# Kernel optimization log

Hardware: AMD Instinct MI355X
Metric: run time of the kernel (lower is better)

## Reference

```python
import jax, jax.numpy as jnp
import numpy as np

N = 100000
E = 1600000
D = 128      # in_features
H = 128      # mlp hidden = out_features
O = 128      # out_features
BN_EPS = 1e-5

def _bn_train(x, gamma, beta):
    # BatchNorm1d in training mode: batch stats over node axis, biased variance
    mu = jnp.mean(x, axis=0)
    var = jnp.mean((x - mu) ** 2, axis=0)
    return (x - mu) * jax.lax.rsqrt(var + BN_EPS) * gamma + beta

def setup_inputs() -> dict:
    key = jax.random.key(0)
    ks = jax.random.split(key, 8)
    h = jax.random.normal(ks[0], (N, D), dtype=jnp.float32)
    edge_src = jax.random.randint(ks[1], (E,), 0, N, dtype=jnp.int32)
    edge_dst = jax.random.randint(ks[2], (E,), 0, N, dtype=jnp.int32)
    s1 = 1.0 / np.sqrt(D)
    s2 = 1.0 / np.sqrt(H)
    W1 = jax.random.uniform(ks[3], (D, H), jnp.float32, -s1, s1)
    b1 = jax.random.uniform(ks[4], (H,), jnp.float32, -s1, s1)
    W2 = jax.random.uniform(ks[5], (H, O), jnp.float32, -s2, s2)
    b2 = jax.random.uniform(ks[6], (O,), jnp.float32, -s2, s2)
    return {
        "h": h, "edge_src": edge_src, "edge_dst": edge_dst,
        "W1": W1, "b1": b1, "g1": jnp.ones((H,), jnp.float32), "be1": jnp.zeros((H,), jnp.float32),
        "W2": W2, "b2": b2, "g2": jnp.ones((O,), jnp.float32), "be2": jnp.zeros((O,), jnp.float32),
        "eps": jnp.zeros((), jnp.float32),
    }

def reference(h, edge_src, edge_dst, W1, b1, g1, be1, W2, b2, g2, be2, eps):
    # spmm(Adj, h) == scatter-add of gathered neighbor features
    msgs = h[edge_src]                                   # [E, D] irregular gather
    pooled = jax.ops.segment_sum(msgs, edge_dst, num_segments=N)  # [N, D]
    pooled = pooled + (1.0 + eps) * h                    # eps combine
    # MLP (2 layers): Linear -> BN -> ReLU -> Linear
    x = jax.nn.relu(_bn_train(pooled @ W1 + b1, g1, be1))
    x = x @ W2 + b2
    # final BN + ReLU
    return jax.nn.relu(_bn_train(x, g2, be2))
```

## Files before the change

### kernel.cpp

```cpp
#include <hip/hip_runtime.h>
#include <hip/hip_bf16.h>
#include <stdint.h>

#define BN_EPS 1e-5f
#define NSTRIPE 64

typedef __attribute__((ext_vector_type(8)))  short bf16x8;
typedef __attribute__((ext_vector_type(16))) float f32x16;

static __device__ __forceinline__ float bflo2f(uint32_t p){
  union { uint32_t u; float f; } c; c.u = p << 16; return c.f;
}
static __device__ __forceinline__ float bfhi2f(uint32_t p){
  union { uint32_t u; float f; } c; c.u = p & 0xffff0000u; return c.f;
}
static __device__ __forceinline__ uint16_t f2bf(float f){
  union { float f; uint32_t u; } c; c.f = f;
  uint32_t u = c.u;
  return (uint16_t)((u + 0x7fffu + ((u >> 16) & 1u)) >> 16);
}
static __device__ __forceinline__ uint32_t pack2(float a, float b){
  return (uint32_t)f2bf(a) | ((uint32_t)f2bf(b) << 16);
}

__global__ void k_prep(const float* __restrict__ h, uint16_t* __restrict__ hb, int hblocks,
                       const float* __restrict__ W1, const float* __restrict__ W2,
                       uint16_t* __restrict__ Wt1, uint16_t* __restrict__ Wt2,
                       float* __restrict__ stats,
                       const int* __restrict__ dst, int* __restrict__ M, int E, int NB){
  int b = blockIdx.x, t = threadIdx.x;
  if (b < hblocks){
    int i = (b * 256 + t) * 8;
    float4 a = *(const float4*)(h + i);
    float4 bb = *(const float4*)(h + i + 4);
    uint4 o;
    o.x = pack2(a.x, a.y); o.y = pack2(a.z, a.w);
    o.z = pack2(bb.x, bb.y); o.w = pack2(bb.z, bb.w);
    *(uint4*)(hb + i) = o;
    return;
  }
  if (b < hblocks + 16){
    int gid = (b - hblocks) * 256 + t;
    {
      float4 z = make_float4(0.f, 0.f, 0.f, 0.f);
      *(float4*)(stats + gid * 8) = z;
      *(float4*)(stats + gid * 8 + 4) = z;
    }
    const float* Wf = (gid < 2048) ? W1 : W2;
    uint16_t* Wt = (gid < 2048) ? Wt1 : Wt2;
    int cid = gid & 2047;
    int nrow = cid >> 4;
    int c    = cid & 15;
    int k0 = c * 8;
    float e[8];
    #pragma unroll
    for (int j = 0; j < 8; ++j) e[j] = Wf[(k0 + j) * 128 + nrow];
    uint4 o;
    o.x = pack2(e[0], e[1]); o.y = pack2(e[2], e[3]);
    o.z = pack2(e[4], e[5]); o.w = pack2(e[6], e[7]);
    *(uint4*)(Wt + nrow * 128 + c * 8) = o;
    return;
  }
  int eb = b - hblocks - 16;
  __shared__ int cnt[512];
  cnt[t] = 0; cnt[t + 256] = 0;
  __syncthreads();
  int base = eb * 4096;
  #pragma unroll 4
  for (int j = t; j < 4096; j += 256){
    int i = base + j;
    if (i < E) atomicAdd(&cnt[dst[i] >> 8], 1);
  }
  __syncthreads();
  size_t row = (size_t)eb * NB;
  if (t < NB) M[row + t] = cnt[t];
  int t2 = t + 256;
  if (t2 < NB) M[row + t2] = cnt[t2];
}

__global__ void k_colscan(int* __restrict__ M, int* __restrict__ btot, int EB, int NB){
  __shared__ int s[256];
  int b = blockIdx.x, t = threadIdx.x;
  int i0 = 2 * t, i1 = 2 * t + 1;
  int v0 = (i0 < EB) ? M[(size_t)i0 * NB + b] : 0;
  int v1 = (i1 < EB) ? M[(size_t)i1 * NB + b] : 0;
  s[t] = v0 + v1;
  __syncthreads();
  for (int off = 1; off < 256; off <<= 1){
    int v = (t >= off) ? s[t - off] : 0;
    __syncthreads();
    s[t] += v;
    __syncthreads();
  }
  int excl = s[t] - (v0 + v1);
  if (i0 < EB) M[(size_t)i0 * NB + b] = excl;
  if (i1 < EB) M[(size_t)i1 * NB + b] = excl + v0;
  if (t == 255) btot[b] = s[255];
}

__global__ void k_bscan(const int* __restrict__ btot, int* __restrict__ bbase,
                        int* __restrict__ row_off, int NB, int n, int E){
  __shared__ int s[256];
  int t = threadIdx.x;
  int i0 = 2 * t, i1 = 2 * t + 1;
  int v0 = (i0 < NB) ? btot[i0] : 0;
  int v1 = (i1 < NB) ? btot[i1] : 0;
  s[t] = v0 + v1;
  __syncthreads();
  for (int off = 1; off < 256; off <<= 1){
    int v = (t >= off) ? s[t - off] : 0;
    __syncthreads();
    s[t] += v;
    __syncthreads();
  }
  int excl = s[t] - (v0 + v1);
  if (i0 < NB) bbase[i0] = excl;
  if (i1 < NB) bbase[i1] = excl + v0;
  if (t == 0){ bbase[NB] = E; row_off[n] = E; }
}

__global__ void k_bin(const int* __restrict__ src, const int* __restrict__ dst,
                      const int* __restrict__ M, const int* __restrict__ bbase,
                      uint2* __restrict__ binned, int E, int NB){
  __shared__ int comb[512];
  __shared__ int cur[512];
  int t = threadIdx.x;
  size_t row = (size_t)blockIdx.x * NB;
  if (t < NB) comb[t] = bbase[t] + M[row + t];
  int t2 = t + 256;
  if (t2 < NB) comb[t2] = bbase[t2] + M[row + t2];
  cur[t] = 0; cur[t + 256] = 0;
  __syncthreads();
  int base = blockIdx.x * 4096;
  #pragma unroll 4
  for (int j = t; j < 4096; j += 256){
    int i = base + j;
    if (i < E){
      int d = dst[i];
      int b = d >> 8;
      int r = atomicAdd(&cur[b], 1);
      binned[comb[b] + r] = make_uint2((unsigned)src[i], (unsigned)d);
    }
  }
}

__global__ void k_csr(const uint2* __restrict__ binned, const int* __restrict__ bbase,
                      int* __restrict__ row_off, int* __restrict__ col_idx, int n){
  __shared__ int cnt[256];
  __shared__ int off[256];
  __shared__ int cur[256];
  int b = blockIdx.x, t = threadIdx.x;
  int e0 = bbase[b], e1 = bbase[b + 1];
  int nb0 = b << 8;
  cnt[t] = 0; cur[t] = 0;
  __syncthreads();
  int m = e1 - e0;
  for (int j = t; j < m; j += 256) atomicAdd(&cnt[binned[e0 + j].y & 255], 1);
  __syncthreads();
  int v = cnt[t];
  off[t] = v;
  __syncthreads();
  for (int o = 1; o < 256; o <<= 1){
    int u = (t >= o) ? off[t - o] : 0;
    __syncthreads();
    off[t] += u;
    __syncthreads();
  }
  int excl = off[t] - v;
  __syncthreads();
  off[t] = excl;
  if (nb0 + t < n) row_off[nb0 + t] = e0 + excl;
  __syncthreads();
  for (int j = t; j < m; j += 256){
    uint2 p = binned[e0 + j];
    int dl = p.y & 255;
    int r = atomicAdd(&cur[dl], 1);
    col_idx[e0 + off[dl] + r] = (int)p.x;
  }
}

__global__ __launch_bounds__(256, 4) void k_gg(
    const uint16_t* __restrict__ hb, const int* __restrict__ row_off,
    const int* __restrict__ col_idx, const float* __restrict__ eps_p,
    const uint16_t* __restrict__ Wt, const float* __restrict__ bias_f,
    uint16_t* __restrict__ Yout, float* __restrict__ osum_s, float* __restrict__ osq_s, int n){
  __shared__ __align__(16) uint16_t Al[64 * 128];
  __shared__ float csum[128], csq[128];
  int tid = threadIdx.x;
  int rbase = blockIdx.x * 64;
  int stripe = blockIdx.x & (NSTRIPE - 1);
  int lane = tid & 63;
  int w    = tid >> 6;
  int g = lane >> 4;
  int c = lane & 15;
  const uint4* hp4 = (const uint4*)hb;
  float ce = 1.0f + eps_p[0];
  if (tid < 128){ csum[tid] = 0.f; csq[tid] = 0.f; }

  for (int it = 0; it < 16; ++it){
    int m = w * 16 + it;
    int gr = rbase + m;
    float a0=0.f,a1=0.f,a2=0.f,a3=0.f,a4=0.f,a5=0.f,a6=0.f,a7=0.f;
    if (gr < n){
      int j = row_off[gr], jend = row_off[gr + 1];
      for (; j + 16 <= jend; j += 16){
        int sA = col_idx[j + g];
        int sB = col_idx[j + 4 + g];
        int sC = col_idx[j + 8 + g];
        int sD = col_idx[j + 12 + g];
        uint4 vA = hp4[(size_t)sA * 16 + c];
        uint4 vB = hp4[(size_t)sB * 16 + c];
        uint4 vC = hp4[(size_t)sC * 16 + c];
        uint4 vD = hp4[(size_t)sD * 16 + c];
        a0 += (bflo2f(vA.x) + bflo2f(vB.x)) + (bflo2f(vC.x) + bflo2f(vD.x));
        a1 += (bfhi2f(vA.x) + bfhi2f(vB.x)) + (bfhi2f(vC.x) + bfhi2f(vD.x));
        a2 += (bflo2f(vA.y) + bflo2f(vB.y)) + (bflo2f(vC.y) + bflo2f(vD.y));
        a3 += (bfhi2f(vA.y) + bfhi2f(vB.y)) + (bfhi2f(vC.y) + bfhi2f(vD.y));
        a4 += (bflo2f(vA.z) + bflo2f(vB.z)) + (bflo2f(vC.z) + bflo2f(vD.z));
        a5 += (bfhi2f(vA.z) + bfhi2f(vB.z)) + (bfhi2f(vC.z) + bfhi2f(vD.z));
        a6 += (bflo2f(vA.w) + bflo2f(vB.w)) + (bflo2f(vC.w) + bflo2f(vD.w));
        a7 += (bfhi2f(vA.w) + bfhi2f(vB.w)) + (bfhi2f(vC.w) + bfhi2f(vD.w));
      }
      for (; j + 4 <= jend; j += 4){
        int s = col_idx[j + g];
        uint4 v = hp4[(size_t)s * 16 + c];
        a0 += bflo2f(v.x); a1 += bfhi2f(v.x);
        a2 += bflo2f(v.y); a3 += bfhi2f(v.y);
        a4 += bflo2f(v.z); a5 += bfhi2f(v.z);
        a6 += bflo2f(v.w); a7 += bfhi2f(v.w);
      }
      int rem = jend - j;
      if (rem > 0){
        int jj = j + (g < rem ? g : rem - 1);
        float wq = (g < rem) ? 1.f : 0.f;
        int s = col_idx[jj];
        uint4 v = hp4[(size_t)s * 16 + c];
        a0 = fmaf(wq, bflo2f(v.x), a0); a1 = fmaf(wq, bfhi2f(v.x), a1);
        a2 = fmaf(wq, bflo2f(v.y), a2); a3 = fmaf(wq, bfhi2f(v.y), a3);
        a4 = fmaf(wq, bflo2f(v.z), a4); a5 = fmaf(wq, bfhi2f(v.z), a5);
        a6 = fmaf(wq, bflo2f(v.w), a6); a7 = fmaf(wq, bfhi2f(v.w), a7);
      }
      a0 += __shfl_xor(a0, 16); a1 += __shfl_xor(a1, 16);
      a2 += __shfl_xor(a2, 16); a3 += __shfl_xor(a3, 16);
      a4 += __shfl_xor(a4, 16); a5 += __shfl_xor(a5, 16);
      a6 += __shfl_xor(a6, 16); a7 += __shfl_xor(a7, 16);
      a0 += __shfl_xor(a0, 32); a1 += __shfl_xor(a1, 32);
      a2 += __shfl_xor(a2, 32); a3 += __shfl_xor(a3, 32);
      a4 += __shfl_xor(a4, 32); a5 += __shfl_xor(a5, 32);
      a6 += __shfl_xor(a6, 32); a7 += __shfl_xor(a7, 32);
      if (g == 0){
        uint4 vh = hp4[(size_t)gr * 16 + c];
        a0 = fmaf(ce, bflo2f(vh.x), a0); a1 = fmaf(ce, bfhi2f(vh.x), a1);
        a2 = fmaf(ce, bflo2f(vh.y), a2); a3 = fmaf(ce, bfhi2f(vh.y), a3);
        a4 = fmaf(ce, bflo2f(vh.z), a4); a5 = fmaf(ce, bfhi2f(vh.z), a5);
        a6 = fmaf(ce, bflo2f(vh.w), a6); a7 = fmaf(ce, bfhi2f(vh.w), a7);
      }
    }
    if (g == 0){
      uint4 o;
      o.x = pack2(a0, a1); o.y = pack2(a2, a3);
      o.z = pack2(a4, a5); o.w = pack2(a6, a7);
      *(uint4*)((char*)Al + m * 256 + ((c ^ (m & 15)) * 16)) = o;
    }
  }
  __syncthreads();

  int hi   = lane >> 5;
  int key  = lane & 15;
  int m0   = (w & 1) * 32;
  int n0   = (w >> 1) * 64;
  int mrow = m0 + (lane & 31);
  int nrow0 = n0 + (lane & 31);
  int nrow1 = nrow0 + 32;

  f32x16 acc0, acc1;
  #pragma unroll
  for (int i = 0; i < 16; ++i){ acc0[i] = 0.f; acc1[i] = 0.f; }

  const char* Ab = (const char*)Al;
  #pragma unroll
  for (int kt = 0; kt < 8; ++kt){
    int ck = 2 * kt + hi;
    bf16x8 a  = *(const bf16x8*)(Ab + mrow * 256 + ((ck ^ key) * 16));
    bf16x8 b0 = *(const bf16x8*)(Wt + nrow0 * 128 + ck * 8);
    bf16x8 b1 = *(const bf16x8*)(Wt + nrow1 * 128 + ck * 8);
    acc0 = __builtin_amdgcn_mfma_f32_32x32x16_bf16(a, b0, acc0, 0, 0, 0);
    acc1 = __builtin_amdgcn_mfma_f32_32x32x16_bf16(a, b1, acc1, 0, 0, 0);
  }
  __syncthreads();

  uint16_t* Yl = Al;
  float bias0 = bias_f[nrow0];
  float bias1 = bias_f[nrow1];
  float ps0 = 0.f, pq0 = 0.f, ps1 = 0.f, pq1 = 0.f;
  #pragma unroll
  for (int r = 0; r < 16; ++r){
    int row = m0 + (r & 3) + 8 * (r >> 2) + 4 * hi;
    bool valid = (rbase + row) < n;
    float y0 = acc0[r] + bias0;
    float y1 = acc1[r] + bias1;
    if (valid){
      ps0 += y0; pq0 += y0 * y0;
      ps1 += y1; pq1 += y1 * y1;
    }
    Yl[row * 128 + nrow0] = f2bf(y0);
    Yl[row * 128 + nrow1] = f2bf(y1);
  }
  atomicAdd(&csum[nrow0], ps0); atomicAdd(&csq[nrow0], pq0);
  atomicAdd(&csum[nrow1], ps1); atomicAdd(&csq[nrow1], pq1);
  __syncthreads();

  #pragma unroll
  for (int i = 0; i < 4; ++i){
    int id = tid + 256 * i;
    int row = id >> 4, cc = id & 15;
    int gr = rbase + row;
    if (gr < n)
      *((uint4*)Yout + (size_t)gr * 16 + cc) = *((const uint4*)Yl + id);
  }
  if (tid < 128){
    atomicAdd(&osum_s[stripe * 128 + tid], csum[tid]);
    atomicAdd(&osq_s[stripe * 128 + tid], csq[tid]);
  }
}

__global__ __launch_bounds__(256, 4) void k_mgemm2(
    const uint16_t* __restrict__ Ag, const uint16_t* __restrict__ Wt,
    const float* __restrict__ bias_f,
    const float* __restrict__ sin_s, const float* __restrict__ sqin_s,
    const float* __restrict__ gin, const float* __restrict__ bein, float invN,
    uint16_t* __restrict__ Yout, float* __restrict__ osum_s, float* __restrict__ osq_s, int n){
  __shared__ __align__(16) uint16_t Al[64 * 128];
  __shared__ float csum[128], csq[128];
  __shared__ __align__(16) float ABl[256];
  int tid = threadIdx.x;
  int rbase = blockIdx.x * 64;
  int stripe = blockIdx.x & (NSTRIPE - 1);

  if (tid < 128){
    float s = 0.f, q = 0.f;
    #pragma unroll 8
    for (int st = 0; st < NSTRIPE; ++st){
      s += sin_s[st * 128 + tid];
      q += sqin_s[st * 128 + tid];
    }
    float mu = s * invN;
    float var = q * invN - mu * mu;
    float A = gin[tid] * rsqrtf(var + BN_EPS);
    ABl[tid] = A;
    ABl[128 + tid] = bein[tid] - mu * A;
    csum[tid] = 0.f; csq[tid] = 0.f;
  }
  __syncthreads();

  #pragma unroll
  for (int i = 0; i < 4; ++i){
    int f = tid + 256 * i;
    int m = f >> 4, c = f & 15;
    int gr = rbase + m;
    uint4 v = make_uint4(0, 0, 0, 0);
    if (gr < n){
      v = *(const uint4*)(Ag + (size_t)gr * 128 + c * 8);
      int k0 = c * 8;
      float4 ka0 = *(const float4*)(ABl + k0);
      float4 ka1 = *(const float4*)(ABl + k0 + 4);
      float4 kb0 = *(const float4*)(ABl + 128 + k0);
      float4 kb1 = *(const float4*)(ABl + 128 + k0 + 4);
      float e0 = fmaxf(fmaf(bflo2f(v.x), ka0.x, kb0.x), 0.f);
      float e1 = fmaxf(fmaf(bfhi2f(v.x), ka0.y, kb0.y), 0.f);
      float e2 = fmaxf(fmaf(bflo2f(v.y), ka0.z, kb0.z), 0.f);
      float e3 = fmaxf(fmaf(bfhi2f(v.y), ka0.w, kb0.w), 0.f);
      float e4 = fmaxf(fmaf(bflo2f(v.z), ka1.x, kb1.x), 0.f);
      float e5 = fmaxf(fmaf(bfhi2f(v.z), ka1.y, kb1.y), 0.f);
      float e6 = fmaxf(fmaf(bflo2f(v.w), ka1.z, kb1.z), 0.f);
      float e7 = fmaxf(fmaf(bfhi2f(v.w), ka1.w, kb1.w), 0.f);
      v.x = pack2(e0, e1); v.y = pack2(e2, e3);
      v.z = pack2(e4, e5); v.w = pack2(e6, e7);
    }
    *(uint4*)((char*)Al + m * 256 + ((c ^ (m & 15)) * 16)) = v;
  }
  __syncthreads();

  int lane = tid & 63;
  int w    = tid >> 6;
  int hi   = lane >> 5;
  int key  = lane & 15;
  int m0   = (w & 1) * 32;
  int n0   = (w >> 1) * 64;
  int mrow = m0 + (lane & 31);
  int nrow0 = n0 + (lane & 31);
  int nrow1 = nrow0 + 32;

  f32x16 acc0, acc1;
  #pragma unroll
  for (int i = 0; i < 16; ++i){ acc0[i] = 0.f; acc1[i] = 0.f; }

  const char* Ab = (const char*)Al;
  #pragma unroll
  for (int kt = 0; kt < 8; ++kt){
    int ck = 2 * kt + hi;
    bf16x8 a  = *(const bf16x8*)(Ab + mrow * 256 + ((ck ^ key) * 16));
    bf16x8 b0 = *(const bf16x8*)(Wt + nrow0 * 128 + ck * 8);
    bf16x8 b1 = *(const bf16x8*)(Wt + nrow1 * 128 + ck * 8);
    acc0 = __builtin_amdgcn_mfma_f32_32x32x16_bf16(a, b0, acc0, 0, 0, 0);
    acc1 = __builtin_amdgcn_mfma_f32_32x32x16_bf16(a, b1, acc1, 0, 0, 0);
  }
  __syncthreads();

  uint16_t* Yl = Al;
  float bias0 = bias_f[nrow0];
  float bias1 = bias_f[nrow1];
  float ps0 = 0.f, pq0 = 0.f, ps1 = 0.f, pq1 = 0.f;
  #pragma unroll
  for (int r = 0; r < 16; ++r){
    int row = m0 + (r & 3) + 8 * (r >> 2) + 4 * hi;
    bool valid = (rbase + row) < n;
    float y0 = acc0[r] + bias0;
    float y1 = acc1[r] + bias1;
    if (valid){
      ps0 += y0; pq0 += y0 * y0;
      ps1 += y1; pq1 += y1 * y1;
    }
    Yl[row * 128 + nrow0] = f2bf(y0);
    Yl[row * 128 + nrow1] = f2bf(y1);
  }
  atomicAdd(&csum[nrow0], ps0); atomicAdd(&csq[nrow0], pq0);
  atomicAdd(&csum[nrow1], ps1); atomicAdd(&csq[nrow1], pq1);
  __syncthreads();

  #pragma unroll
  for (int i = 0; i < 4; ++i){
    int id = tid + 256 * i;
    int row = id >> 4, cc = id & 15;
    int gr = rbase + row;
    if (gr < n)
      *((uint4*)Yout + (size_t)gr * 16 + cc) = *((const uint4*)Yl + id);
  }
  if (tid < 128){
    atomicAdd(&osum_s[stripe * 128 + tid], csum[tid]);
    atomicAdd(&osq_s[stripe * 128 + tid], csq[tid]);
  }
}

__global__ void k_bncoef2(const float* __restrict__ sum_s, const float* __restrict__ sq_s,
                          const float* __restrict__ g, const float* __restrict__ be,
                          float* __restrict__ AB, float invN){
  int c = threadIdx.x;
  if (c < 128){
    float s = 0.f, q = 0.f;
    #pragma unroll 8
    for (int st = 0; st < NSTRIPE; ++st){
      s += sum_s[st * 128 + c];
      q += sq_s[st * 128 + c];
    }
    float mu = s * invN;
    float var = q * invN - mu * mu;
    float A = g[c] * rsqrtf(var + BN_EPS);
    AB[c] = A;
    AB[128 + c] = be[c] - mu * A;
  }
}

__global__ void k_final(const uint16_t* __restrict__ Y2b, const float* __restrict__ ABg,
                        float* __restrict__ out, int total){
  __shared__ __align__(16) float AB[256];
  int tid = threadIdx.x;
  if (tid < 64){
    *(float4*)(AB + tid * 4) = *(const float4*)(ABg + tid * 4);
  }
  __syncthreads();
  int i = (blockIdx.x * 256 + tid) * 4;
  if (i >= total) return;
  uint2 v = *(const uint2*)(Y2b + i);
  int c = i & 127;
  float4 a = *(const float4*)(AB + c);
  float4 b = *(const float4*)(AB + 128 + c);
  float4 o;
  o.x = fmaxf(fmaf(bflo2f(v.x), a.x, b.x), 0.f);
  o.y = fmaxf(fmaf(bfhi2f(v.x), a.y, b.y), 0.f);
  o.z = fmaxf(fmaf(bflo2f(v.y), a.z, b.z), 0.f);
  o.w = fmaxf(fmaf(bfhi2f(v.y), a.w, b.w), 0.f);
  *(float4*)(out + i) = o;
}

extern "C" void kernel_launch(void* const* d_in, const int* in_sizes, int n_in,
                              void* d_out, int out_size, void* d_ws, size_t ws_size,
                              hipStream_t stream){
  const float* h    = (const float*)d_in[0];
  const int*   esrc = (const int*)d_in[1];
  const int*   edst = (const int*)d_in[2];
  const float* W1   = (const float*)d_in[3];
  const float* b1   = (const float*)d_in[4];
  const float* g1   = (const float*)d_in[5];
  const float* be1  = (const float*)d_in[6];
  const float* W2   = (const float*)d_in[7];
  const float* b2   = (const float*)d_in[8];
  const float* g2   = (const float*)d_in[9];
  const float* be2  = (const float*)d_in[10];
  const float* eps  = (const float*)d_in[11];
  int n = in_sizes[0] / 128;
  int E = in_sizes[1];
  (void)n_in; (void)out_size; (void)ws_size;

  int NB = (n + 255) >> 8;
  int EB = (E + 4095) >> 12;

  char* ws = (char*)d_ws;
  size_t off = 0;
  auto alloc = [&](size_t bytes) -> void* {
    void* p = ws + off;
    off += (bytes + 511) & ~(size_t)511;
    return p;
  };
  size_t feat_b = (size_t)n * 128 * 2;
  uint16_t* B1   = (uint16_t*)alloc(feat_b);
  uint16_t* B2   = (uint16_t*)alloc(feat_b);
  int*   row_off = (int*)alloc((size_t)(n + 1) * 4);
  int*   col_idx = (int*)alloc((size_t)E * 4);
  int*   M       = (int*)alloc((size_t)EB * NB * 4);
  int*   btot    = (int*)alloc((size_t)(NB + 1) * 4);
  int*   bbase   = (int*)alloc((size_t)(NB + 1) * 4);
  float* stats   = (float*)alloc((size_t)4 * NSTRIPE * 128 * 4);
  float* AB2     = (float*)alloc(256 * 4);
  uint16_t* Wt1  = (uint16_t*)alloc(128 * 128 * 2);
  uint16_t* Wt2  = (uint16_t*)alloc(128 * 128 * 2);
  float* sum1 = stats;
  float* sq1  = stats + NSTRIPE * 128;
  float* sum2 = stats + 2 * NSTRIPE * 128;
  float* sq2  = stats + 3 * NSTRIPE * 128;
  uint16_t* hb  = B1;
  uint2*   binned = (uint2*)B2;
  uint16_t* Y1b = B2;
  uint16_t* Y2b = B1;

  int total = n * 128;
  int hblocks = total / 8 / 256;
  float invN = 1.0f / (float)n;

  k_prep<<<hblocks + 16 + EB, 256, 0, stream>>>(h, hb, hblocks, W1, W2, Wt1, Wt2,
                                                stats, edst, M, E, NB);
  k_colscan<<<NB, 256, 0, stream>>>(M, btot, EB, NB);
  k_bscan  <<<1, 256, 0, stream>>>(btot, bbase, row_off, NB, n, E);
  k_bin    <<<EB, 256, 0, stream>>>(esrc, edst, M, bbase, binned, E, NB);
  k_csr    <<<NB, 256, 0, stream>>>(binned, bbase, row_off, col_idx, n);

  int gblocks = (n + 63) / 64;
  k_gg<<<gblocks, 256, 0, stream>>>(hb, row_off, col_idx, eps, Wt1, b1,
                                    Y1b, sum1, sq1, n);
  k_mgemm2<<<gblocks, 256, 0, stream>>>(Y1b, Wt2, b2,
      sum1, sq1, g1, be1, invN, Y2b, sum2, sq2, n);

  k_bncoef2<<<1, 128, 0, stream>>>(sum2, sq2, g2, be2, AB2, invN);
  k_final<<<(total / 4 + 255) / 256, 256, 0, stream>>>(Y2b, AB2, (float*)d_out, total);
}
```

Before: 305.2 us.

## Pack binned edges into 32-bit words and assign one 16-lane group per row

The binned edge array now packs the source index (24 bits) and the low 8 bits of the destination into one 32-bit word instead of a uint2, halving the binning write and CSR read traffic. The gather kernel now gives each 16-lane group its own destination row, so 16 rows are in flight per block iteration instead of 4. Each group issues eight independent row gathers per loop step, and the cross-group shuffle reduction and g==0 predication are gone. In exchange, all 16 lanes load the same col_idx entries redundantly, and rows with fewer edges leave lanes idle in the masked tail. The 24-bit packing limits node count to 16M.

```diff
diff --git a/kernel.cpp b/kernel.cpp
--- a/kernel.cpp
+++ b/kernel.cpp
@@ -121,7 +121,7 @@
 
 __global__ void k_bin(const int* __restrict__ src, const int* __restrict__ dst,
                       const int* __restrict__ M, const int* __restrict__ bbase,
-                      uint2* __restrict__ binned, int E, int NB){
+                      uint32_t* __restrict__ binned, int E, int NB){
   __shared__ int comb[512];
   __shared__ int cur[512];
   int t = threadIdx.x;
@@ -139,12 +139,12 @@
       int d = dst[i];
       int b = d >> 8;
       int r = atomicAdd(&cur[b], 1);
-      binned[comb[b] + r] = make_uint2((unsigned)src[i], (unsigned)d);
-    }
-  }
-}
-
-__global__ void k_csr(const uint2* __restrict__ binned, const int* __restrict__ bbase,
+      binned[comb[b] + r] = (uint32_t)src[i] | ((uint32_t)(d & 255) << 24);
+    }
+  }
+}
+
+__global__ void k_csr(const uint32_t* __restrict__ binned, const int* __restrict__ bbase,
                       int* __restrict__ row_off, int* __restrict__ col_idx, int n){
   __shared__ int cnt[256];
   __shared__ int off[256];
@@ -155,7 +155,7 @@
   cnt[t] = 0; cur[t] = 0;
   __syncthreads();
   int m = e1 - e0;
-  for (int j = t; j < m; j += 256) atomicAdd(&cnt[binned[e0 + j].y & 255], 1);
+  for (int j = t; j < m; j += 256) atomicAdd(&cnt[binned[e0 + j] >> 24], 1);
   __syncthreads();
   int v = cnt[t];
   off[t] = v;
@@ -172,10 +172,10 @@
   if (nb0 + t < n) row_off[nb0 + t] = e0 + excl;
   __syncthreads();
   for (int j = t; j < m; j += 256){
-    uint2 p = binned[e0 + j];
-    int dl = p.y & 255;
+    uint32_t p = binned[e0 + j];
+    int dl = (int)(p >> 24);
     int r = atomicAdd(&cur[dl], 1);
-    col_idx[e0 + off[dl] + r] = (int)p.x;
+    col_idx[e0 + off[dl] + r] = (int)(p & 0xFFFFFFu);
   }
 }
 
@@ -189,82 +189,67 @@
   int tid = threadIdx.x;
   int rbase = blockIdx.x * 64;
   int stripe = blockIdx.x & (NSTRIPE - 1);
-  int lane = tid & 63;
-  int w    = tid >> 6;
-  int g = lane >> 4;
-  int c = lane & 15;
+  int grp = tid >> 4;
+  int c   = tid & 15;
   const uint4* hp4 = (const uint4*)hb;
   float ce = 1.0f + eps_p[0];
   if (tid < 128){ csum[tid] = 0.f; csq[tid] = 0.f; }
 
-  for (int it = 0; it < 16; ++it){
-    int m = w * 16 + it;
+  for (int it = 0; it < 4; ++it){
+    int m = it * 16 + grp;
     int gr = rbase + m;
     float a0=0.f,a1=0.f,a2=0.f,a3=0.f,a4=0.f,a5=0.f,a6=0.f,a7=0.f;
     if (gr < n){
       int j = row_off[gr], jend = row_off[gr + 1];
-      for (; j + 16 <= jend; j += 16){
-        int sA = col_idx[j + g];
-        int sB = col_idx[j + 4 + g];
-        int sC = col_idx[j + 8 + g];
-        int sD = col_idx[j + 12 + g];
-        uint4 vA = hp4[(size_t)sA * 16 + c];
-        uint4 vB = hp4[(size_t)sB * 16 + c];
-        uint4 vC = hp4[(size_t)sC * 16 + c];
-        uint4 vD = hp4[(size_t)sD * 16 + c];
-        a0 += (bflo2f(vA.x) + bflo2f(vB.x)) + (bflo2f(vC.x) + bflo2f(vD.x));
-        a1 += (bfhi2f(vA.x) + bfhi2f(vB.x)) + (bfhi2f(vC.x) + bfhi2f(vD.x));
-        a2 += (bflo2f(vA.y) + bflo2f(vB.y)) + (bflo2f(vC.y) + bflo2f(vD.y));
-        a3 += (bfhi2f(vA.y) + bfhi2f(vB.y)) + (bfhi2f(vC.y) + bfhi2f(vD.y));
-        a4 += (bflo2f(vA.z) + bflo2f(vB.z)) + (bflo2f(vC.z) + bflo2f(vD.z));
-        a5 += (bfhi2f(vA.z) + bfhi2f(vB.z)) + (bfhi2f(vC.z) + bfhi2f(vD.z));
-        a6 += (bflo2f(vA.w) + bflo2f(vB.w)) + (bflo2f(vC.w) + bflo2f(vD.w));
-        a7 += (bfhi2f(vA.w) + bfhi2f(vB.w)) + (bfhi2f(vC.w) + bfhi2f(vD.w));
+      for (; j + 8 <= jend; j += 8){
+        int s[8];
+        #pragma unroll
+        for (int e = 0; e < 8; ++e) s[e] = col_idx[j + e];
+        uint4 v[8];
+        #pragma unroll
+        for (int e = 0; e < 8; ++e) v[e] = hp4[(size_t)s[e] * 16 + c];
+        #pragma unroll
+        for (int e = 0; e < 8; ++e){
+          a0 += bflo2f(v[e].x); a1 += bfhi2f(v[e].x);
+          a2 += bflo2f(v[e].y); a3 += bfhi2f(v[e].y);
+          a4 += bflo2f(v[e].z); a5 += bfhi2f(v[e].z);
+          a6 += bflo2f(v[e].w); a7 += bfhi2f(v[e].w);
+        }
       }
-      for (; j + 4 <= jend; j += 4){
-        int s = col_idx[j + g];
-        uint4 v = hp4[(size_t)s * 16 + c];
-        a0 += bflo2f(v.x); a1 += bfhi2f(v.x);
-        a2 += bflo2f(v.y); a3 += bfhi2f(v.y);
-        a4 += bflo2f(v.z); a5 += bfhi2f(v.z);
-        a6 += bflo2f(v.w); a7 += bfhi2f(v.w);
+      if (j < jend){
+        int s[8]; float wq[8];
+        #pragma unroll
+        for (int e = 0; e < 8; ++e){
+          int jj = j + e;
+          wq[e] = (jj < jend) ? 1.f : 0.f;
+          s[e] = col_idx[(jj < jend) ? jj : (jend - 1)];
+        }
+        uint4 v[8];
+        #pragma unroll
+        for (int e = 0; e < 8; ++e) v[e] = hp4[(size_t)s[e] * 16 + c];
+        #pragma unroll
+        for (int e = 0; e < 8; ++e){
+          a0 = fmaf(wq[e], bflo2f(v[e].x), a0); a1 = fmaf(wq[e], bfhi2f(v[e].x), a1);
+          a2 = fmaf(wq[e], bflo2f(v[e].y), a2); a3 = fmaf(wq[e], bfhi2f(v[e].y), a3);
+          a4 = fmaf(wq[e], bflo2f(v[e].z), a4); a5 = fmaf(wq[e], bfhi2f(v[e].z), a5);
+          a6 = fmaf(wq[e], bflo2f(v[e].w), a6); a7 = fmaf(wq[e], bfhi2f(v[e].w), a7);
+        }
       }
-      int rem = jend - j;
-      if (rem > 0){
-        int jj = j + (g < rem ? g : rem - 1);
-        float wq = (g < rem) ? 1.f : 0.f;
-        int s = col_idx[jj];
-        uint4 v = hp4[(size_t)s * 16 + c];
-        a0 = fmaf(wq, bflo2f(v.x), a0); a1 = fmaf(wq, bfhi2f(v.x), a1);
-        a2 = fmaf(wq, bflo2f(v.y), a2); a3 = fmaf(wq, bfhi2f(v.y), a3);
-        a4 = fmaf(wq, bflo2f(v.z), a4); a5 = fmaf(wq, bfhi2f(v.z), a5);
-        a6 = fmaf(wq, bflo2f(v.w), a6); a7 = fmaf(wq, bfhi2f(v.w), a7);
-      }
-      a0 += __shfl_xor(a0, 16); a1 += __shfl_xor(a1, 16);
-      a2 += __shfl_xor(a2, 16); a3 += __shfl_xor(a3, 16);
-      a4 += __shfl_xor(a4, 16); a5 += __shfl_xor(a5, 16);
-      a6 += __shfl_xor(a6, 16); a7 += __shfl_xor(a7, 16);
-      a0 += __shfl_xor(a0, 32); a1 += __shfl_xor(a1, 32);
-      a2 += __shfl_xor(a2, 32); a3 += __shfl_xor(a3, 32);
-      a4 += __shfl_xor(a4, 32); a5 += __shfl_xor(a5, 32);
-      a6 += __shfl_xor(a6, 32); a7 += __shfl_xor(a7, 32);
-      if (g == 0){
-        uint4 vh = hp4[(size_t)gr * 16 + c];
-        a0 = fmaf(ce, bflo2f(vh.x), a0); a1 = fmaf(ce, bfhi2f(vh.x), a1);
-        a2 = fmaf(ce, bflo2f(vh.y), a2); a3 = fmaf(ce, bfhi2f(vh.y), a3);
-        a4 = fmaf(ce, bflo2f(vh.z), a4); a5 = fmaf(ce, bfhi2f(vh.z), a5);
-        a6 = fmaf(ce, bflo2f(vh.w), a6); a7 = fmaf(ce, bfhi2f(vh.w), a7);
-      }
-    }
-    if (g == 0){
-      uint4 o;
-      o.x = pack2(a0, a1); o.y = pack2(a2, a3);
-      o.z = pack2(a4, a5); o.w = pack2(a6, a7);
-      *(uint4*)((char*)Al + m * 256 + ((c ^ (m & 15)) * 16)) = o;
-    }
-  }
-  __syncthreads();
-
+      uint4 vh = hp4[(size_t)gr * 16 + c];
+      a0 = fmaf(ce, bflo2f(vh.x), a0); a1 = fmaf(ce, bfhi2f(vh.x), a1);
+      a2 = fmaf(ce, bflo2f(vh.y), a2); a3 = fmaf(ce, bfhi2f(vh.y), a3);
+      a4 = fmaf(ce, bflo2f(vh.z), a4); a5 = fmaf(ce, bfhi2f(vh.z), a5);
+      a6 = fmaf(ce, bflo2f(vh.w), a6); a7 = fmaf(ce, bfhi2f(vh.w), a7);
+    }
+    uint4 o;
+    o.x = pack2(a0, a1); o.y = pack2(a2, a3);
+    o.z = pack2(a4, a5); o.w = pack2(a6, a7);
+    *(uint4*)((char*)Al + m * 256 + ((c ^ (m & 15)) * 16)) = o;
+  }
+  __syncthreads();
+
+  int lane = tid & 63;
+  int w    = tid >> 6;
   int hi   = lane >> 5;
   int key  = lane & 15;
   int m0   = (w & 1) * 32;
@@ -529,7 +514,7 @@
   float* sum2 = stats + 2 * NSTRIPE * 128;
   float* sq2  = stats + 3 * NSTRIPE * 128;
   uint16_t* hb  = B1;
-  uint2*   binned = (uint2*)B2;
+  uint32_t* binned = (uint32_t*)B2;
   uint16_t* Y1b = B2;
   uint16_t* Y2b = B1;
 
```

After: 300.4 us. About the same (-1.6%).
